# Optimization experiments

Measured on AMD Instinct MI355X. Metric: run time of the kernel, lower is better.

The kernel has to match this reference:

```python
import jax, jax.numpy as jnp
import numpy as np

N_NODES = 50000
N_EDGES = 1600000
F_IN = 32
F_OUT = 32


def setup_inputs() -> dict:
    key = jax.random.key(0)
    k1, k2, k3, k4, k5 = jax.random.split(key, 5)
    inputs = jax.random.normal(k1, (N_EDGES, F_IN), dtype=jnp.float32)
    src = jax.random.randint(k2, (N_EDGES,), 0, N_NODES, dtype=jnp.int32)
    dst = jax.random.randint(k3, (N_EDGES,), 0, N_NODES, dtype=jnp.int32)
    W = jax.random.normal(k4, (F_OUT, F_IN), dtype=jnp.float32) * (1.0 / np.sqrt(F_IN))
    b = jax.random.normal(k5, (F_OUT,), dtype=jnp.float32) * 0.01
    return {"inputs": inputs, "src": src, "dst": dst, "W": W, "b": b}


def reference(inputs, src, dst, W, b):
    # Step 1: node h = mean of incoming edge features (mean over in-edges).
    ones = jnp.ones((inputs.shape[0],), dtype=inputs.dtype)
    in_deg = jax.ops.segment_sum(ones, dst, num_segments=N_NODES)  # [N]
    node_sum = jax.ops.segment_sum(inputs, dst, num_segments=N_NODES)  # [N, F]
    node_mean = node_sum / jnp.maximum(in_deg, 1.0)[:, None]
    # Step 2: send_and_recv: msg = src node h; reduce = sum at dst node.
    node_h = jax.ops.segment_sum(node_mean[src], dst, num_segments=N_NODES)  # [N, F]
    # Step 3: edge h = mean of its two endpoint node features.
    edge_h = 0.5 * (node_h[src] + node_h[dst])  # [E, F]
    # Step 4: final linear projection on edge features.
    return edge_h @ W.T + b
```

## Files before the change

### kernel.cpp

```cpp
#include <hip/hip_runtime.h>

#define N_NODES 50000
#define N_EDGES 1600000
#define F 32
#define BSH 7
#define BSIZE (1 << BSH)
#define NB ((N_NODES + BSIZE - 1) >> BSH)
#define FILL_CHUNK 8192
#define EMASK 0x1FFFFF

__global__ __launch_bounds__(256)
void k_bhist(const int* __restrict__ dst, int* __restrict__ bhist) {
    __shared__ int lh[NB];
    for (int i = threadIdx.x; i < NB; i += 256) lh[i] = 0;
    __syncthreads();
    for (int e = blockIdx.x * blockDim.x + threadIdx.x; e < N_EDGES;
         e += gridDim.x * blockDim.x)
        atomicAdd(&lh[dst[e] >> BSH], 1);
    __syncthreads();
    for (int i = threadIdx.x; i < NB; i += 256)
        if (lh[i]) atomicAdd(&bhist[i], lh[i]);
}

__global__ __launch_bounds__(512)
void k_bscan(const int* __restrict__ bhist,
             int* __restrict__ bucket_off,
             int* __restrict__ cursor) {
    __shared__ int s[512];
    int t = threadIdx.x;
    int v = (t < NB) ? bhist[t] : 0;
    s[t] = v;
    __syncthreads();
    for (int off = 1; off < 512; off <<= 1) {
        int u = (t >= off) ? s[t - off] : 0;
        __syncthreads();
        s[t] += u;
        __syncthreads();
    }
    if (t < NB) {
        int ex = s[t] - v;
        bucket_off[t] = ex;
        cursor[t] = ex;
    }
    if (t == NB - 1) bucket_off[NB] = s[t];
}

__global__ __launch_bounds__(256)
void k_coarse_fill(const int* __restrict__ dst,
                   const int* __restrict__ src,
                   int* __restrict__ cursor,
                   int2* __restrict__ coarse2) {
    __shared__ int lh[NB];
    __shared__ int gb[NB];
    int lo = blockIdx.x * FILL_CHUNK;
    int hi = min(lo + FILL_CHUNK, N_EDGES);

    for (int i = threadIdx.x; i < NB; i += 256) lh[i] = 0;
    __syncthreads();
    for (int e = lo + threadIdx.x; e < hi; e += 256)
        atomicAdd(&lh[dst[e] >> BSH], 1);
    __syncthreads();
    for (int i = threadIdx.x; i < NB; i += 256) {
        gb[i] = atomicAdd(&cursor[i], lh[i]);
        lh[i] = 0;
    }
    __syncthreads();
    for (int e = lo + threadIdx.x; e < hi; e += 256) {
        int d = dst[e];
        int bk = d >> BSH;
        int r = atomicAdd(&lh[bk], 1);
        int2 v;
        v.x = e | ((d & (BSIZE - 1)) << 21);
        v.y = src[e];
        coarse2[gb[bk] + r] = v;
    }
}

__global__ __launch_bounds__(256)
void k_exact_fill(const int2* __restrict__ coarse2,
                  const int* __restrict__ bucket_off,
                  int* __restrict__ row_off,
                  int* __restrict__ eid_sorted,
                  int* __restrict__ src_sorted) {
    __shared__ int cnt[BSIZE];
    __shared__ int s[BSIZE];
    __shared__ int cur[BSIZE];
    int tid = threadIdx.x;
    int b = blockIdx.x;
    int lo = bucket_off[b], hi = bucket_off[b + 1];

    if (tid < BSIZE) cnt[tid] = 0;
    __syncthreads();
    for (int i = lo + tid; i < hi; i += 256)
        atomicAdd(&cnt[(coarse2[i].x >> 21) & (BSIZE - 1)], 1);
    __syncthreads();
    if (tid < BSIZE) s[tid] = cnt[tid];
    __syncthreads();
    for (int off = 1; off < BSIZE; off <<= 1) {
        int v = 0;
        if (tid < BSIZE && tid >= off) v = s[tid - off];
        __syncthreads();
        if (tid < BSIZE) s[tid] += v;
        __syncthreads();
    }
    int nbase = b << BSH;
    if (tid < BSIZE) {
        int base = lo + s[tid] - cnt[tid];
        cur[tid] = base;
        if (nbase + tid < N_NODES) row_off[nbase + tid] = base;
    }
    if (b == NB - 1 && tid == 0) row_off[N_NODES] = N_EDGES;
    __syncthreads();
    for (int i = lo + tid; i < hi; i += 256) {
        int2 v = coarse2[i];
        int l = (v.x >> 21) & (BSIZE - 1);
        int p = atomicAdd(&cur[l], 1);
        eid_sorted[p] = v.x & EMASK;
        src_sorted[p] = v.y;
    }
}

__global__ __launch_bounds__(256)
void k_node_mean(const float* __restrict__ inputs,
                 const int* __restrict__ eid_sorted,
                 const int* __restrict__ row_off,
                 float* __restrict__ node_mean) {
    int wave = (blockIdx.x * blockDim.x + threadIdx.x) >> 6;
    if (wave >= N_NODES) return;
    int lane  = threadIdx.x & 63;
    int eslot = lane >> 3;
    int q     = lane & 7;

    int s0 = row_off[wave];
    int s1 = row_off[wave + 1];

    float4 acc = {0.f, 0.f, 0.f, 0.f};
    for (int i = s0 + eslot; i < s1; i += 8) {
        int e = eid_sorted[i];
        float4 v = *reinterpret_cast<const float4*>(&inputs[(size_t)e * F + q * 4]);
        acc.x += v.x; acc.y += v.y; acc.z += v.z; acc.w += v.w;
    }
    #pragma unroll
    for (int m = 8; m <= 32; m <<= 1) {
        acc.x += __shfl_xor(acc.x, m);
        acc.y += __shfl_xor(acc.y, m);
        acc.z += __shfl_xor(acc.z, m);
        acc.w += __shfl_xor(acc.w, m);
    }
    if (eslot == 0) {
        float r = 1.0f / fmaxf((float)(s1 - s0), 1.0f);
        float4 o = {acc.x * r, acc.y * r, acc.z * r, acc.w * r};
        *reinterpret_cast<float4*>(&node_mean[(size_t)wave * F + q * 4]) = o;
    }
}

__global__ __launch_bounds__(256)
void k_node_h_project(const int* __restrict__ src_sorted,
                      const int* __restrict__ row_off,
                      const float* __restrict__ node_mean,
                      const float* __restrict__ W,
                      float* __restrict__ node_p) {
    __shared__ float Wl[32][33];
    __shared__ float hr[4][36];

    int tid = threadIdx.x;
    #pragma unroll
    for (int i = tid; i < 1024; i += 256) Wl[i >> 5][i & 31] = W[i];

    int wv    = tid >> 6;
    int lane  = tid & 63;
    int eslot = lane >> 3;
    int q     = lane & 7;
    int n     = blockIdx.x * 4 + wv;

    int s0 = row_off[n];
    int s1 = row_off[n + 1];

    float4 acc = {0.f, 0.f, 0.f, 0.f};
    for (int i = s0 + eslot; i < s1; i += 8) {
        int s = src_sorted[i];
        float4 v = *reinterpret_cast<const float4*>(&node_mean[(size_t)s * F + q * 4]);
        acc.x += v.x; acc.y += v.y; acc.z += v.z; acc.w += v.w;
    }
    #pragma unroll
    for (int m = 8; m <= 32; m <<= 1) {
        acc.x += __shfl_xor(acc.x, m);
        acc.y += __shfl_xor(acc.y, m);
        acc.z += __shfl_xor(acc.z, m);
        acc.w += __shfl_xor(acc.w, m);
    }
    if (eslot == 0) {
        *reinterpret_cast<float4*>(&hr[wv][q * 4]) = acc;
    }
    __syncthreads();

    if (tid < 128) {
        int ln = tid >> 5;
        int o  = tid & 31;
        float sacc = 0.f;
        #pragma unroll
        for (int i = 0; i < 32; ++i) sacc += hr[ln][i] * Wl[o][i];
        node_p[(size_t)(blockIdx.x * 4 + ln) * F + o] = sacc;
    }
}

__global__ void k_edge_out(const int* __restrict__ src,
                           const int* __restrict__ dst,
                           const float* __restrict__ node_p,
                           const float* __restrict__ b,
                           float* __restrict__ out) {
    int tid = blockIdx.x * blockDim.x + threadIdx.x;
    if (tid >= N_EDGES * 8) return;
    int e = tid >> 3;
    int q = tid & 7;
    int s = src[e];
    int d = dst[e];

    const float4 a  = *reinterpret_cast<const float4*>(&node_p[(size_t)s * F + q * 4]);
    const float4 c  = *reinterpret_cast<const float4*>(&node_p[(size_t)d * F + q * 4]);
    const float4 bb = *reinterpret_cast<const float4*>(&b[q * 4]);

    float4 r;
    r.x = 0.5f * (a.x + c.x) + bb.x;
    r.y = 0.5f * (a.y + c.y) + bb.y;
    r.z = 0.5f * (a.z + c.z) + bb.z;
    r.w = 0.5f * (a.w + c.w) + bb.w;

    *reinterpret_cast<float4*>(&out[(size_t)e * F + q * 4]) = r;
}

extern "C" void kernel_launch(void* const* d_in, const int* in_sizes, int n_in,
                              void* d_out, int out_size, void* d_ws, size_t ws_size,
                              hipStream_t stream) {
    const float* inputs = (const float*)d_in[0];
    const int*   src    = (const int*)d_in[1];
    const int*   dst    = (const int*)d_in[2];
    const float* W      = (const float*)d_in[3];
    const float* b      = (const float*)d_in[4];
    float* out = (float*)d_out;

    float* node_mean = (float*)d_ws;
    float* node_p    = node_mean + (size_t)N_NODES * F;
    int2* coarse2    = (int2*)(node_p + (size_t)N_NODES * F);
    int*  bhist      = (int*)(coarse2 + N_EDGES);
    int*  bucket_off = bhist + NB;
    int*  cursor     = bucket_off + NB + 1;
    int*  row_off    = cursor + NB;
    int*  eid_sorted = row_off + N_NODES + 1;
    int*  src_sorted = eid_sorted + N_EDGES;

    hipMemsetAsync(bhist, 0, NB * sizeof(int), stream);

    k_bhist<<<256, 256, 0, stream>>>(dst, bhist);
    k_bscan<<<1, 512, 0, stream>>>(bhist, bucket_off, cursor);
    k_coarse_fill<<<(N_EDGES + FILL_CHUNK - 1) / FILL_CHUNK, 256, 0, stream>>>(
        dst, src, cursor, coarse2);
    k_exact_fill<<<NB, 256, 0, stream>>>(
        coarse2, bucket_off, row_off, eid_sorted, src_sorted);

    int node_blocks = (N_NODES + 3) / 4;
    k_node_mean<<<node_blocks, 256, 0, stream>>>(inputs, eid_sorted, row_off, node_mean);
    k_node_h_project<<<N_NODES / 4, 256, 0, stream>>>(
        src_sorted, row_off, node_mean, W, node_p);
    k_edge_out<<<(N_EDGES * 8 + 255) / 256, 256, 0, stream>>>(src, dst, node_p, b, out);
}
```

Measured before the change: 255.4 us.

## Narrow src indices to 16-bit, add nontemporal loads/stores and index prefetch

Splits the packed int2 coarse buffer into an int edge-id array plus a 16-bit source-node array, and stores sorted sources as 16-bit, cutting index traffic in the sort and gather stages. It adds nontemporal loads for streamed inputs and indices and a nontemporal store for the output. The gather loops software-prefetch the next index, and the fill chunk size is halved to launch more blocks. Node IDs up to 50000 fit in unsigned short, so this relies on N_NODES staying below 65536.

```diff
diff --git a/kernel.cpp b/kernel.cpp
--- a/kernel.cpp
+++ b/kernel.cpp
@@ -6,8 +6,17 @@
 #define BSH 7
 #define BSIZE (1 << BSH)
 #define NB ((N_NODES + BSIZE - 1) >> BSH)
-#define FILL_CHUNK 8192
+#define FILL_CHUNK 4096
 #define EMASK 0x1FFFFF
+
+typedef float f4 __attribute__((ext_vector_type(4)));
+
+__device__ __forceinline__ f4 nt_load4(const float* p) {
+    return __builtin_nontemporal_load((const f4*)p);
+}
+__device__ __forceinline__ int nt_loadi(const int* p) {
+    return __builtin_nontemporal_load(p);
+}
 
 __global__ __launch_bounds__(256)
 void k_bhist(const int* __restrict__ dst, int* __restrict__ bhist) {
@@ -16,7 +25,7 @@
     __syncthreads();
     for (int e = blockIdx.x * blockDim.x + threadIdx.x; e < N_EDGES;
          e += gridDim.x * blockDim.x)
-        atomicAdd(&lh[dst[e] >> BSH], 1);
+        atomicAdd(&lh[nt_loadi(&dst[e]) >> BSH], 1);
     __syncthreads();
     for (int i = threadIdx.x; i < NB; i += 256)
         if (lh[i]) atomicAdd(&bhist[i], lh[i]);
@@ -49,7 +58,8 @@
 void k_coarse_fill(const int* __restrict__ dst,
                    const int* __restrict__ src,
                    int* __restrict__ cursor,
-                   int2* __restrict__ coarse2) {
+                   int* __restrict__ coarseE,
+                   unsigned short* __restrict__ coarseS) {
     __shared__ int lh[NB];
     __shared__ int gb[NB];
     int lo = blockIdx.x * FILL_CHUNK;
@@ -58,7 +68,7 @@
     for (int i = threadIdx.x; i < NB; i += 256) lh[i] = 0;
     __syncthreads();
     for (int e = lo + threadIdx.x; e < hi; e += 256)
-        atomicAdd(&lh[dst[e] >> BSH], 1);
+        atomicAdd(&lh[nt_loadi(&dst[e]) >> BSH], 1);
     __syncthreads();
     for (int i = threadIdx.x; i < NB; i += 256) {
         gb[i] = atomicAdd(&cursor[i], lh[i]);
@@ -69,19 +79,19 @@
         int d = dst[e];
         int bk = d >> BSH;
         int r = atomicAdd(&lh[bk], 1);
-        int2 v;
-        v.x = e | ((d & (BSIZE - 1)) << 21);
-        v.y = src[e];
-        coarse2[gb[bk] + r] = v;
-    }
-}
-
-__global__ __launch_bounds__(256)
-void k_exact_fill(const int2* __restrict__ coarse2,
+        int p = gb[bk] + r;
+        coarseE[p] = e | ((d & (BSIZE - 1)) << 21);
+        coarseS[p] = (unsigned short)src[e];
+    }
+}
+
+__global__ __launch_bounds__(256)
+void k_exact_fill(const int* __restrict__ coarseE,
+                  const unsigned short* __restrict__ coarseS,
                   const int* __restrict__ bucket_off,
                   int* __restrict__ row_off,
                   int* __restrict__ eid_sorted,
-                  int* __restrict__ src_sorted) {
+                  unsigned short* __restrict__ src_sorted) {
     __shared__ int cnt[BSIZE];
     __shared__ int s[BSIZE];
     __shared__ int cur[BSIZE];
@@ -92,7 +102,7 @@
     if (tid < BSIZE) cnt[tid] = 0;
     __syncthreads();
     for (int i = lo + tid; i < hi; i += 256)
-        atomicAdd(&cnt[(coarse2[i].x >> 21) & (BSIZE - 1)], 1);
+        atomicAdd(&cnt[(coarseE[i] >> 21) & (BSIZE - 1)], 1);
     __syncthreads();
     if (tid < BSIZE) s[tid] = cnt[tid];
     __syncthreads();
@@ -112,11 +122,11 @@
     if (b == NB - 1 && tid == 0) row_off[N_NODES] = N_EDGES;
     __syncthreads();
     for (int i = lo + tid; i < hi; i += 256) {
-        int2 v = coarse2[i];
-        int l = (v.x >> 21) & (BSIZE - 1);
+        int ev = coarseE[i];
+        int l = (ev >> 21) & (BSIZE - 1);
         int p = atomicAdd(&cur[l], 1);
-        eid_sorted[p] = v.x & EMASK;
-        src_sorted[p] = v.y;
+        eid_sorted[p] = ev & EMASK;
+        src_sorted[p] = coarseS[i];
     }
 }
 
@@ -134,11 +144,15 @@
     int s0 = row_off[wave];
     int s1 = row_off[wave + 1];
 
-    float4 acc = {0.f, 0.f, 0.f, 0.f};
-    for (int i = s0 + eslot; i < s1; i += 8) {
-        int e = eid_sorted[i];
-        float4 v = *reinterpret_cast<const float4*>(&inputs[(size_t)e * F + q * 4]);
-        acc.x += v.x; acc.y += v.y; acc.z += v.z; acc.w += v.w;
+    f4 acc = {0.f, 0.f, 0.f, 0.f};
+    int i = s0 + eslot;
+    int e = (i < s1) ? eid_sorted[i] : 0;
+    while (i < s1) {
+        int inext = i + 8;
+        int enext = (inext < s1) ? eid_sorted[inext] : 0;
+        f4 v = nt_load4(&inputs[(size_t)e * F + q * 4]);
+        acc += v;
+        i = inext; e = enext;
     }
     #pragma unroll
     for (int m = 8; m <= 32; m <<= 1) {
@@ -149,13 +163,13 @@
     }
     if (eslot == 0) {
         float r = 1.0f / fmaxf((float)(s1 - s0), 1.0f);
-        float4 o = {acc.x * r, acc.y * r, acc.z * r, acc.w * r};
-        *reinterpret_cast<float4*>(&node_mean[(size_t)wave * F + q * 4]) = o;
-    }
-}
-
-__global__ __launch_bounds__(256)
-void k_node_h_project(const int* __restrict__ src_sorted,
+        f4 o = acc * r;
+        *reinterpret_cast<f4*>(&node_mean[(size_t)wave * F + q * 4]) = o;
+    }
+}
+
+__global__ __launch_bounds__(256)
+void k_node_h_project(const unsigned short* __restrict__ src_sorted,
                       const int* __restrict__ row_off,
                       const float* __restrict__ node_mean,
                       const float* __restrict__ W,
@@ -176,11 +190,15 @@
     int s0 = row_off[n];
     int s1 = row_off[n + 1];
 
-    float4 acc = {0.f, 0.f, 0.f, 0.f};
-    for (int i = s0 + eslot; i < s1; i += 8) {
-        int s = src_sorted[i];
-        float4 v = *reinterpret_cast<const float4*>(&node_mean[(size_t)s * F + q * 4]);
-        acc.x += v.x; acc.y += v.y; acc.z += v.z; acc.w += v.w;
+    f4 acc = {0.f, 0.f, 0.f, 0.f};
+    int i = s0 + eslot;
+    int s = (i < s1) ? (int)src_sorted[i] : 0;
+    while (i < s1) {
+        int inext = i + 8;
+        int snext = (inext < s1) ? (int)src_sorted[inext] : 0;
+        f4 v = *reinterpret_cast<const f4*>(&node_mean[(size_t)s * F + q * 4]);
+        acc += v;
+        i = inext; s = snext;
     }
     #pragma unroll
     for (int m = 8; m <= 32; m <<= 1) {
@@ -190,7 +208,7 @@
         acc.w += __shfl_xor(acc.w, m);
     }
     if (eslot == 0) {
-        *reinterpret_cast<float4*>(&hr[wv][q * 4]) = acc;
+        *reinterpret_cast<f4*>(&hr[wv][q * 4]) = acc;
     }
     __syncthreads();
 
@@ -199,34 +217,30 @@
         int o  = tid & 31;
         float sacc = 0.f;
         #pragma unroll
-        for (int i = 0; i < 32; ++i) sacc += hr[ln][i] * Wl[o][i];
+        for (int i2 = 0; i2 < 32; ++i2) sacc += hr[ln][i2] * Wl[o][i2];
         node_p[(size_t)(blockIdx.x * 4 + ln) * F + o] = sacc;
     }
 }
 
-__global__ void k_edge_out(const int* __restrict__ src,
-                           const int* __restrict__ dst,
-                           const float* __restrict__ node_p,
-                           const float* __restrict__ b,
-                           float* __restrict__ out) {
+__global__ __launch_bounds__(256)
+void k_edge_out(const int* __restrict__ src,
+                const int* __restrict__ dst,
+                const float* __restrict__ node_p,
+                const float* __restrict__ b,
+                float* __restrict__ out) {
     int tid = blockIdx.x * blockDim.x + threadIdx.x;
     if (tid >= N_EDGES * 8) return;
     int e = tid >> 3;
     int q = tid & 7;
-    int s = src[e];
-    int d = dst[e];
-
-    const float4 a  = *reinterpret_cast<const float4*>(&node_p[(size_t)s * F + q * 4]);
-    const float4 c  = *reinterpret_cast<const float4*>(&node_p[(size_t)d * F + q * 4]);
-    const float4 bb = *reinterpret_cast<const float4*>(&b[q * 4]);
-
-    float4 r;
-    r.x = 0.5f * (a.x + c.x) + bb.x;
-    r.y = 0.5f * (a.y + c.y) + bb.y;
-    r.z = 0.5f * (a.z + c.z) + bb.z;
-    r.w = 0.5f * (a.w + c.w) + bb.w;
-
-    *reinterpret_cast<float4*>(&out[(size_t)e * F + q * 4]) = r;
+    int s = nt_loadi(&src[e]);
+    int d = nt_loadi(&dst[e]);
+
+    const f4 a  = *reinterpret_cast<const f4*>(&node_p[(size_t)s * F + q * 4]);
+    const f4 c  = *reinterpret_cast<const f4*>(&node_p[(size_t)d * F + q * 4]);
+    const f4 bb = *reinterpret_cast<const f4*>(&b[q * 4]);
+
+    f4 r = 0.5f * (a + c) + bb;
+    __builtin_nontemporal_store(r, (f4*)&out[(size_t)e * F + q * 4]);
 }
 
 extern "C" void kernel_launch(void* const* d_in, const int* in_sizes, int n_in,
@@ -241,22 +255,23 @@
 
     float* node_mean = (float*)d_ws;
     float* node_p    = node_mean + (size_t)N_NODES * F;
-    int2* coarse2    = (int2*)(node_p + (size_t)N_NODES * F);
-    int*  bhist      = (int*)(coarse2 + N_EDGES);
+    int*  coarseE    = (int*)(node_p + (size_t)N_NODES * F);
+    int*  eid_sorted = coarseE + N_EDGES;
+    int*  bhist      = eid_sorted + N_EDGES;
     int*  bucket_off = bhist + NB;
     int*  cursor     = bucket_off + NB + 1;
     int*  row_off    = cursor + NB;
-    int*  eid_sorted = row_off + N_NODES + 1;
-    int*  src_sorted = eid_sorted + N_EDGES;
+    unsigned short* coarseS    = (unsigned short*)(row_off + N_NODES + 1);
+    unsigned short* src_sorted = coarseS + N_EDGES;
 
     hipMemsetAsync(bhist, 0, NB * sizeof(int), stream);
 
     k_bhist<<<256, 256, 0, stream>>>(dst, bhist);
     k_bscan<<<1, 512, 0, stream>>>(bhist, bucket_off, cursor);
     k_coarse_fill<<<(N_EDGES + FILL_CHUNK - 1) / FILL_CHUNK, 256, 0, stream>>>(
-        dst, src, cursor, coarse2);
+        dst, src, cursor, coarseE, coarseS);
     k_exact_fill<<<NB, 256, 0, stream>>>(
-        coarse2, bucket_off, row_off, eid_sorted, src_sorted);
+        coarseE, coarseS, bucket_off, row_off, eid_sorted, src_sorted);
 
     int node_blocks = (N_NODES + 3) / 4;
     k_node_mean<<<node_blocks, 256, 0, stream>>>(inputs, eid_sorted, row_off, node_mean);
```

After: 260.4 us. Within noise of the previous version (+2.0%).
